# Kernel optimization log

Hardware: AMD Instinct MI355X
Metric: run time of the kernel (lower is better)

## Reference

```python
import jax, jax.numpy as jnp
import numpy as np

DIM = 1024
HEADS = 16
HEAD_DIM = DIM // HEADS // 2  # 32
DEPTH = 12
LAMBDA_INIT = 0.8 - 0.6 * float(np.exp(-0.3 * DEPTH))
EPS = 1e-5
B, N = 2, 2048


def setup_inputs() -> dict:
    key = jax.random.key(0)
    ks = jax.random.split(key, 9)
    s = 0.02
    return {
        "x": jax.random.normal(ks[0], (B, N, DIM), jnp.float32),
        "W_qkv": jax.random.normal(ks[1], (DIM, 3 * DIM), jnp.float32) * s,
        "W_proj": jax.random.normal(ks[2], (DIM, DIM), jnp.float32) * s,
        "b_proj": jnp.zeros((DIM,), jnp.float32),
        "lambda_q1": jax.random.normal(ks[3], (HEAD_DIM,), jnp.float32) * 0.1,
        "lambda_k1": jax.random.normal(ks[4], (HEAD_DIM,), jnp.float32) * 0.1,
        "lambda_q2": jax.random.normal(ks[5], (HEAD_DIM,), jnp.float32) * 0.1,
        "lambda_k2": jax.random.normal(ks[6], (HEAD_DIM,), jnp.float32) * 0.1,
        "subln_w": jnp.ones((2 * HEAD_DIM,), jnp.float32),
    }


def reference(x, W_qkv, W_proj, b_proj, lambda_q1, lambda_k1, lambda_q2, lambda_k2, subln_w):
    Bm, Nm, C = x.shape
    H, hd = HEADS, HEAD_DIM
    scale = hd ** -0.5

    qkv = (x @ W_qkv).reshape(Bm, Nm, 3, H, 2 * hd)
    q, k, v = qkv[:, :, 0], qkv[:, :, 1], qkv[:, :, 2]
    # split each head's 2*hd dims into two sub-heads -> [B, 2H, N, hd]
    q = q.reshape(Bm, Nm, 2 * H, hd).transpose(0, 2, 1, 3)
    k = k.reshape(Bm, Nm, 2 * H, hd).transpose(0, 2, 1, 3)
    v = v.transpose(0, 2, 1, 3)  # [B, H, N, 2*hd]

    q1, q2 = q[:, :H], q[:, H:]
    k1, k2 = k[:, :H], k[:, H:]

    def sdpa(qh, kh):
        scores = jnp.einsum('bhqd,bhkd->bhqk', qh, kh) * scale
        a = jax.nn.softmax(scores, axis=-1)
        return jnp.einsum('bhqk,bhkd->bhqd', a, v)  # [B,H,N,2*hd]

    attn1 = sdpa(q1, k1)
    attn2 = sdpa(q2, k2)

    lam1 = jnp.exp(jnp.sum(lambda_q1 * lambda_k1))
    lam2 = jnp.exp(jnp.sum(lambda_q2 * lambda_k2))
    lam = lam1 - lam2 + LAMBDA_INIT

    o = attn1 - lam * attn2  # [B,H,N,2*hd]
    # RMSNorm over last dim (2*hd) with elementwise affine
    o = o * jax.lax.rsqrt(jnp.mean(o * o, axis=-1, keepdims=True) + EPS)
    o = o * subln_w
    o = o * (1.0 - LAMBDA_INIT)

    o = o.transpose(0, 2, 1, 3).reshape(Bm, Nm, C)
    return o @ W_proj + b_proj
```

## Files before the change

kernel.cpp:

```cpp
#include <hip/hip_runtime.h>

typedef unsigned short ushort_t;
typedef unsigned int uint_t;
typedef __attribute__((ext_vector_type(4))) float f32x4;
typedef __attribute__((ext_vector_type(8))) __bf16 bf16x8;

#define LAMBDA_INIT 0.7836057665316245f
#define ONE_MINUS_LI 0.21639423346837552f
#define QSCALE_LOG2E 0.25505654442552663f

__device__ inline ushort_t f2bf(float f) {
  union { float f; unsigned u; } v; v.f = f;
  unsigned r = (v.u + 0x7FFFu + ((v.u >> 16) & 1u)) >> 16;
  return (ushort_t)r;
}

__device__ inline float fexp2(float x) {
  float r;
  asm("v_exp_f32 %0, %1" : "=v"(r) : "v"(x));
  return r;
}

__device__ inline uint_t cvtpk(float lo, float hi) {
  uint_t r;
  asm("v_cvt_pk_bf16_f32 %0, %1, %2" : "=v"(r) : "v"(lo), "v"(hi));
  return r;
}

__device__ inline f32x4 zero4() { f32x4 z = {0.f, 0.f, 0.f, 0.f}; return z; }

__device__ inline f32x4 mfma16(bf16x8 a, bf16x8 b, f32x4 c) {
  return __builtin_amdgcn_mfma_f32_16x16x32_bf16(a, b, c, 0, 0, 0);
}

__device__ inline void gload_lds16(const void* g, void* l) {
  __builtin_amdgcn_global_load_lds(
      (const __attribute__((address_space(1))) unsigned int*)g,
      (__attribute__((address_space(3))) unsigned int*)l, 16, 0, 0);
}

__global__ __launch_bounds__(256) void cvt_f32_bf16(const float* __restrict__ in,
                                                    ushort_t* __restrict__ out, int n) {
  int i = (blockIdx.x * 256 + threadIdx.x) * 8;
  if (i >= n) return;
  float4 a = *(const float4*)(in + i);
  float4 b = *(const float4*)(in + i + 4);
  uint4 pack;
  pack.x = cvtpk(a.x, a.y);
  pack.y = cvtpk(a.z, a.w);
  pack.z = cvtpk(b.x, b.y);
  pack.w = cvtpk(b.z, b.w);
  *(uint4*)(out + i) = pack;
}

__global__ __launch_bounds__(256) void transpose_to_bf16(const float* __restrict__ W,
                                                         ushort_t* __restrict__ WT,
                                                         int K, int N) {
  __shared__ float tile[32][33];
  int n0 = blockIdx.x * 32, k0 = blockIdx.y * 32;
  int tx = threadIdx.x & 31, ty = threadIdx.x >> 5;
#pragma unroll
  for (int j = 0; j < 4; ++j) {
    int k = k0 + ty + j * 8;
    tile[ty + j * 8][tx] = W[(size_t)k * N + n0 + tx];
  }
  __syncthreads();
#pragma unroll
  for (int j = 0; j < 4; ++j) {
    int n = n0 + ty + j * 8;
    WT[(size_t)n * K + k0 + tx] = f2bf(tile[tx][ty + j * 8]);
  }
}

template <int MODE>
__global__ __launch_bounds__(256) void gemm_bt(const ushort_t* __restrict__ A,
                                               const ushort_t* __restrict__ Bt,
                                               void* __restrict__ C,
                                               ushort_t* __restrict__ vt_out,
                                               const float* __restrict__ bias,
                                               int M, int N, int K) {
  __shared__ ushort_t As[128 * 32];
  __shared__ ushort_t Bs[128 * 32];
  const int tid = threadIdx.x;
  const int wave = tid >> 6, lane = tid & 63;
  const int wr = wave >> 1, wc = wave & 1;
  const int lg = lane >> 4, ll = lane & 15;

  const int lin = blockIdx.x + gridDim.x * blockIdx.y;
  const int cpx = (gridDim.x * gridDim.y) >> 3;
  const int swz = (lin & 7) * cpx + (lin >> 3);
  const int row0 = (swz % gridDim.x) * 128, col0 = (swz / gridDim.x) * 128;

  f32x4 acc[4][4];
#pragma unroll
  for (int m = 0; m < 4; ++m)
#pragma unroll
    for (int n = 0; n < 4; ++n) acc[m][n] = zero4();

  for (int k0 = 0; k0 < K; k0 += 32) {
    __syncthreads();
#pragma unroll
    for (int i = 0; i < 2; ++i) {
      int c = tid + i * 256;
      int r = c >> 2, ko = (c & 3) << 3;
      gload_lds16(A + (size_t)(row0 + r) * K + k0 + ko,
                  (char*)As + (size_t)(wave * 64 + i * 256) * 16);
      gload_lds16(Bt + (size_t)(col0 + r) * K + k0 + ko,
                  (char*)Bs + (size_t)(wave * 64 + i * 256) * 16);
    }
    __syncthreads();
    bf16x8 af[4], bf[4];
#pragma unroll
    for (int m = 0; m < 4; ++m)
      af[m] = *(const bf16x8*)(As + (wr * 64 + m * 16 + ll) * 32 + (lg << 3));
#pragma unroll
    for (int n = 0; n < 4; ++n)
      bf[n] = *(const bf16x8*)(Bs + (wc * 64 + n * 16 + ll) * 32 + (lg << 3));
#pragma unroll
    for (int m = 0; m < 4; ++m)
#pragma unroll
      for (int n = 0; n < 4; ++n) acc[m][n] = mfma16(af[m], bf[n], acc[m][n]);
  }

#pragma unroll
  for (int m = 0; m < 4; ++m) {
#pragma unroll
    for (int n = 0; n < 4; ++n) {
      int gc = col0 + wc * 64 + n * 16 + ll;
      int gr0 = row0 + wr * 64 + m * 16 + (lg << 2);
      if (MODE == 0) {
#pragma unroll
        for (int j = 0; j < 4; ++j)
          ((float*)C)[(size_t)(gr0 + j) * N + gc] = acc[m][n][j] + bias[gc];
      } else {
        if (gc < 2048) {
          float sc = (gc < 1024) ? QSCALE_LOG2E : 1.0f;
#pragma unroll
          for (int j = 0; j < 4; ++j)
            ((ushort_t*)C)[(size_t)(gr0 + j) * 2048 + gc] = f2bf(acc[m][n][j] * sc);
        } else {
          int hv = (gc - 2048) >> 6, dv = (gc - 2048) & 63;
          int bb = gr0 >> 11, nn = gr0 & 2047;
          uint2 w;
          w.x = cvtpk(acc[m][n][0], acc[m][n][1]);
          w.y = cvtpk(acc[m][n][2], acc[m][n][3]);
          *(uint2*)(vt_out + ((size_t)((bb * 16 + hv) * 64 + dv)) * 2048 + nn) = w;
        }
      }
    }
  }
}

__global__ __launch_bounds__(256) void diff_attn(const ushort_t* __restrict__ qk,
                                                 const ushort_t* __restrict__ vt,
                                                 ushort_t* __restrict__ o,
                                                 const float* __restrict__ lq1,
                                                 const float* __restrict__ lk1,
                                                 const float* __restrict__ lq2,
                                                 const float* __restrict__ lk2,
                                                 const float* __restrict__ subln) {
  const int lin = blockIdx.x + (blockIdx.y << 5) + (blockIdx.z << 9);
  const int swz = ((lin & 7) << 7) + (lin >> 3);
  const int qt = swz & 31, h = (swz >> 5) & 15, b = swz >> 9;
  const int tid = threadIdx.x, wave = tid >> 6, lane = tid & 63;
  const int lg = lane >> 4, ll = lane & 15;

  const size_t qbase = (size_t)b * 2048 * 2048;
  const int cq1 = (h << 5), cq2 = 512 + (h << 5);
  const int ck1 = 1024 + (h << 5), ck2 = 1536 + (h << 5);
  const size_t vbase = (size_t)((b * 16 + h) * 64) * 2048;

  float sl1 = 0.f, sl2 = 0.f;
  for (int j = 0; j < 32; ++j) { sl1 += lq1[j] * lk1[j]; sl2 += lq2[j] * lk2[j]; }
  const float lam = __expf(sl1) - __expf(sl2) + LAMBDA_INIT;

  __shared__ ushort_t Ks[2][64 * 64];
  __shared__ ushort_t Vs[2][64 * 64];
  __shared__ ushort_t Pl[4][16 * 72];

  const int qrow = qt * 64 + wave * 16 + ll;
  const bf16x8 q1f = *(const bf16x8*)(qk + qbase + (size_t)qrow * 2048 + cq1 + (lg << 3));
  const bf16x8 q2f = *(const bf16x8*)(qk + qbase + (size_t)qrow * 2048 + cq2 + (lg << 3));

  f32x4 o1[4], o2[4];
#pragma unroll
  for (int nb = 0; nb < 4; ++nb) { o1[nb] = zero4(); o2[nb] = zero4(); }
  float l1p = 0.f, l2p = 0.f;
  ushort_t* Pw = &Pl[wave][0];

  const int s0 = tid, s1 = tid + 256;
  const int r0 = s0 >> 3, c0 = (s0 & 7) ^ (r0 & 7);
  const int r1 = s1 >> 3, c1 = (s1 & 7) ^ (r1 & 7);
  const int kc0 = ((c0 & 4) ? ck2 : ck1) + ((c0 & 3) << 3);
  const int kc1 = ((c1 & 4) ? ck2 : ck1) + ((c1 & 3) << 3);
  const int ub0 = (wave << 6) * 16;
  const int ub1 = ((wave << 6) + 256) * 16;

#define STAGE(buf, kv0)                                                                   \
  do {                                                                                    \
    gload_lds16(qk + qbase + (size_t)((kv0) + r0) * 2048 + kc0, (char*)Ks[buf] + ub0);    \
    gload_lds16(qk + qbase + (size_t)((kv0) + r1) * 2048 + kc1, (char*)Ks[buf] + ub1);    \
    gload_lds16(vt + vbase + (size_t)r0 * 2048 + (kv0) + (c0 << 3), (char*)Vs[buf] + ub0);\
    gload_lds16(vt + vbase + (size_t)r1 * 2048 + (kv0) + (c1 << 3), (char*)Vs[buf] + ub1);\
  } while (0)

  auto compute_tile = [&](const ushort_t* Kc, const ushort_t* Vc) {
    bf16x8 vf[2][4];
#pragma unroll
    for (int ks = 0; ks < 2; ++ks)
#pragma unroll
      for (int nb = 0; nb < 4; ++nb)
        vf[ks][nb] = *(const bf16x8*)(Vc + nb * 1024 + ll * 64 + (((ks * 4 + lg) ^ (ll & 7)) << 3));
#pragma unroll
    for (int pass = 0; pass < 2; ++pass) {
      const int cK = (lg ^ (ll & 7)) ^ (pass << 2);
      bf16x8 kf[4];
#pragma unroll
      for (int nb = 0; nb < 4; ++nb)
        kf[nb] = *(const bf16x8*)(Kc + nb * 1024 + ll * 64 + (cK << 3));
      const bf16x8 qf = pass ? q2f : q1f;
      f32x4* oacc = pass ? o2 : o1;
      f32x4 s[4];
#pragma unroll
      for (int nb = 0; nb < 4; ++nb)
        s[nb] = mfma16(kf[nb], qf, zero4());
      float part = 0.f;
#pragma unroll
      for (int nb = 0; nb < 4; ++nb) {
        float e0 = fexp2(s[nb][0]), e1 = fexp2(s[nb][1]);
        float e2 = fexp2(s[nb][2]), e3 = fexp2(s[nb][3]);
        part += (e0 + e1) + (e2 + e3);
        uint2 w;
        w.x = cvtpk(e0, e1);
        w.y = cvtpk(e2, e3);
        *(uint2*)(Pw + ll * 72 + nb * 16 + (lg << 2)) = w;
      }
      if (pass) l2p += part; else l1p += part;
#pragma unroll
      for (int ks = 0; ks < 2; ++ks) {
        bf16x8 pf = *(const bf16x8*)(Pw + ll * 72 + ks * 32 + (lg << 3));
#pragma unroll
        for (int nb = 0; nb < 4; ++nb) oacc[nb] = mfma16(pf, vf[ks][nb], oacc[nb]);
      }
    }
  };

  STAGE(0, 0);
  __syncthreads();
  for (int tt = 0; tt < 16; ++tt) {
    STAGE(1, (tt * 2 + 1) * 64);
    compute_tile(Ks[0], Vs[0]);
    __syncthreads();
    if (tt < 15) STAGE(0, (tt * 2 + 2) * 64);
    compute_tile(Ks[1], Vs[1]);
    __syncthreads();
  }
#undef STAGE

  float l1 = l1p; l1 += __shfl_xor(l1, 16); l1 += __shfl_xor(l1, 32);
  float l2 = l2p; l2 += __shfl_xor(l2, 16); l2 += __shfl_xor(l2, 32);
  float i1[4], i2[4];
#pragma unroll
  for (int j = 0; j < 4; ++j) {
    int src = (lane & 48) | ((lg << 2) + j);
    i1[j] = 1.f / __shfl(l1, src);
    i2[j] = 1.f / __shfl(l2, src);
  }

  float ss[4] = {0.f, 0.f, 0.f, 0.f};
  f32x4 ov[4];
#pragma unroll
  for (int nb = 0; nb < 4; ++nb) {
#pragma unroll
    for (int j = 0; j < 4; ++j) {
      float x = o1[nb][j] * i1[j] - lam * (o2[nb][j] * i2[j]);
      ov[nb][j] = x;
      ss[j] += x * x;
    }
  }
#pragma unroll
  for (int mask = 1; mask < 16; mask <<= 1)
#pragma unroll
    for (int j = 0; j < 4; ++j) ss[j] += __shfl_xor(ss[j], mask);
  float nf[4];
#pragma unroll
  for (int j = 0; j < 4; ++j) nf[j] = rsqrtf(ss[j] * (1.f / 64.f) + 1e-5f);
  const size_t orow0 = (size_t)(b * 2048 + qt * 64 + wave * 16);
#pragma unroll
  for (int nb = 0; nb < 4; ++nb) {
    int d = nb * 16 + ll;
    float sw = subln[d] * ONE_MINUS_LI;
#pragma unroll
    for (int j = 0; j < 4; ++j) {
      int r = (lg << 2) + j;
      o[(orow0 + r) * 1024 + (h << 6) + d] = f2bf(ov[nb][j] * nf[j] * sw);
    }
  }
}

extern "C" void kernel_launch(void* const* d_in, const int* in_sizes, int n_in,
                              void* d_out, int out_size, void* d_ws, size_t ws_size,
                              hipStream_t stream) {
  const float* x      = (const float*)d_in[0];
  const float* W_qkv  = (const float*)d_in[1];
  const float* W_proj = (const float*)d_in[2];
  const float* b_proj = (const float*)d_in[3];
  const float* lq1    = (const float*)d_in[4];
  const float* lk1    = (const float*)d_in[5];
  const float* lq2    = (const float*)d_in[6];
  const float* lk2    = (const float*)d_in[7];
  const float* subln  = (const float*)d_in[8];

  char* ws = (char*)d_ws;
  ushort_t* xb     = (ushort_t*)(ws);
  ushort_t* qkb    = (ushort_t*)(ws + 8388608);
  ushort_t* vtb    = (ushort_t*)(ws + 25165824);
  ushort_t* wqkvT  = (ushort_t*)(ws + 33554432);
  ushort_t* wprojT = (ushort_t*)(ws + 39845888);
  ushort_t* ob     = (ushort_t*)(ws + 41943040);

  cvt_f32_bf16<<<2048, 256, 0, stream>>>(x, xb, 4096 * 1024);
  transpose_to_bf16<<<dim3(96, 32), 256, 0, stream>>>(W_qkv, wqkvT, 1024, 3072);
  transpose_to_bf16<<<dim3(32, 32), 256, 0, stream>>>(W_proj, wprojT, 1024, 1024);
  gemm_bt<1><<<dim3(32, 24), 256, 0, stream>>>(xb, wqkvT, (void*)qkb, vtb, nullptr, 4096, 3072, 1024);
  diff_attn<<<dim3(32, 16, 2), 256, 0, stream>>>(qkb, vtb, ob, lq1, lk1, lq2, lk2, subln);
  gemm_bt<0><<<dim3(32, 8), 256, 0, stream>>>(ob, wprojT, d_out, nullptr, b_proj, 4096, 1024, 1024);
}
```

Baseline: 171.7 us.

## Single-buffer V in LDS via register prefetch and add MFMA priority hints

V now has one LDS buffer instead of two. Each tile's V fragments are read into registers before the next V tile is staged into the same buffer, which frees LDS and could allow more blocks per CU. s_setprio hints are also placed around the QK and PV MFMA groups so waves issuing matrix ops get scheduling priority. In exchange the loop gains an extra __syncthreads per tile, and V fragments held in registers raise register pressure.

```diff
diff --git a/kernel.cpp b/kernel.cpp
--- a/kernel.cpp
+++ b/kernel.cpp
@@ -175,7 +175,7 @@
   const float lam = __expf(sl1) - __expf(sl2) + LAMBDA_INIT;
 
   __shared__ ushort_t Ks[2][64 * 64];
-  __shared__ ushort_t Vs[2][64 * 64];
+  __shared__ ushort_t Vs[64 * 64];
   __shared__ ushort_t Pl[4][16 * 72];
 
   const int qrow = qt * 64 + wave * 16 + ll;
@@ -196,21 +196,26 @@
   const int ub0 = (wave << 6) * 16;
   const int ub1 = ((wave << 6) + 256) * 16;
 
-#define STAGE(buf, kv0)                                                                   \
+#define STAGE_K(buf, kv0)                                                                 \
   do {                                                                                    \
     gload_lds16(qk + qbase + (size_t)((kv0) + r0) * 2048 + kc0, (char*)Ks[buf] + ub0);    \
     gload_lds16(qk + qbase + (size_t)((kv0) + r1) * 2048 + kc1, (char*)Ks[buf] + ub1);    \
-    gload_lds16(vt + vbase + (size_t)r0 * 2048 + (kv0) + (c0 << 3), (char*)Vs[buf] + ub0);\
-    gload_lds16(vt + vbase + (size_t)r1 * 2048 + (kv0) + (c1 << 3), (char*)Vs[buf] + ub1);\
   } while (0)
-
-  auto compute_tile = [&](const ushort_t* Kc, const ushort_t* Vc) {
-    bf16x8 vf[2][4];
+#define STAGE_V(kv0)                                                                      \
+  do {                                                                                    \
+    gload_lds16(vt + vbase + (size_t)r0 * 2048 + (kv0) + (c0 << 3), (char*)Vs + ub0);     \
+    gload_lds16(vt + vbase + (size_t)r1 * 2048 + (kv0) + (c1 << 3), (char*)Vs + ub1);     \
+  } while (0)
+
+  auto read_vf = [&](bf16x8 (&vf)[2][4]) {
 #pragma unroll
     for (int ks = 0; ks < 2; ++ks)
 #pragma unroll
       for (int nb = 0; nb < 4; ++nb)
-        vf[ks][nb] = *(const bf16x8*)(Vc + nb * 1024 + ll * 64 + (((ks * 4 + lg) ^ (ll & 7)) << 3));
+        vf[ks][nb] = *(const bf16x8*)(Vs + nb * 1024 + ll * 64 + (((ks * 4 + lg) ^ (ll & 7)) << 3));
+  };
+
+  auto compute_tile = [&](const ushort_t* Kc, const bf16x8 (&vf)[2][4]) {
 #pragma unroll
     for (int pass = 0; pass < 2; ++pass) {
       const int cK = (lg ^ (ll & 7)) ^ (pass << 2);
@@ -221,9 +226,11 @@
       const bf16x8 qf = pass ? q2f : q1f;
       f32x4* oacc = pass ? o2 : o1;
       f32x4 s[4];
+      __builtin_amdgcn_s_setprio(1);
 #pragma unroll
       for (int nb = 0; nb < 4; ++nb)
         s[nb] = mfma16(kf[nb], qf, zero4());
+      __builtin_amdgcn_s_setprio(0);
       float part = 0.f;
 #pragma unroll
       for (int nb = 0; nb < 4; ++nb) {
@@ -236,26 +243,40 @@
         *(uint2*)(Pw + ll * 72 + nb * 16 + (lg << 2)) = w;
       }
       if (pass) l2p += part; else l1p += part;
+      __builtin_amdgcn_s_setprio(1);
 #pragma unroll
       for (int ks = 0; ks < 2; ++ks) {
         bf16x8 pf = *(const bf16x8*)(Pw + ll * 72 + ks * 32 + (lg << 3));
 #pragma unroll
         for (int nb = 0; nb < 4; ++nb) oacc[nb] = mfma16(pf, vf[ks][nb], oacc[nb]);
       }
+      __builtin_amdgcn_s_setprio(0);
     }
   };
 
-  STAGE(0, 0);
+  STAGE_K(0, 0);
+  STAGE_V(0);
   __syncthreads();
-  for (int tt = 0; tt < 16; ++tt) {
-    STAGE(1, (tt * 2 + 1) * 64);
-    compute_tile(Ks[0], Vs[0]);
-    __syncthreads();
-    if (tt < 15) STAGE(0, (tt * 2 + 2) * 64);
-    compute_tile(Ks[1], Vs[1]);
-    __syncthreads();
-  }
-#undef STAGE
+  for (int it = 0; it < 16; ++it) {
+    const int t0 = it * 2;
+    bf16x8 vf[2][4];
+    read_vf(vf);
+    __syncthreads();
+    STAGE_V((t0 + 1) * 64);
+    STAGE_K(1, (t0 + 1) * 64);
+    compute_tile(Ks[0], vf);
+    __syncthreads();
+    read_vf(vf);
+    __syncthreads();
+    if (it < 15) {
+      STAGE_V((t0 + 2) * 64);
+      STAGE_K(0, (t0 + 2) * 64);
+    }
+    compute_tile(Ks[1], vf);
+    __syncthreads();
+  }
+#undef STAGE_K
+#undef STAGE_V
 
   float l1 = l1p; l1 += __shfl_xor(l1, 16); l1 += __shfl_xor(l1, 32);
   float l2 = l2p; l2 += __shfl_xor(l2, 16); l2 += __shfl_xor(l2, 32);
```

Measured after the change: 173.0 us. No clear change (+0.8%).
